# Optimization experiments

Hardware: AMD Instinct MI355X
Metric: run time of the kernel (lower is better)

The kernel has to match this reference:

```python
import jax, jax.numpy as jnp
import numpy as np

B, S, DIM = 2, 2048, 2048
H = 16
Q_LORA, KV_LORA = 768, 512
NOPE, ROPE, VD = 128, 64, 128
QKD = NOPE + ROPE  # 192
SOFTCAP = 30.0
EPS = 1e-6
NEG = -1e9
SCALE = QKD ** -0.5  # max_seq_len <= original_seq_len -> no mscale correction


def rms_norm(x, w, eps=EPS):
    xf = x.astype(jnp.float32)
    y = xf * jax.lax.rsqrt(jnp.mean(xf * xf, axis=-1, keepdims=True) + eps)
    return (y * w.astype(jnp.float32)).astype(x.dtype)


def apply_rope(x, cos, sin):
    # x: [B, S, H, D] with interleaved (even, odd) pairs; cos/sin: [S, D//2]
    xr = x.astype(jnp.float32).reshape(*x.shape[:-1], -1, 2)
    xe, xo = xr[..., 0], xr[..., 1]
    c = cos[None, :, None, :]
    s = sin[None, :, None, :]
    ye = xe * c - xo * s
    yo = xe * s + xo * c
    return jnp.stack([ye, yo], axis=-1).reshape(x.shape).astype(x.dtype)


def setup_inputs():
    key = jax.random.key(0)
    ks = jax.random.split(key, 6)
    def w(k, shape, fan_in):
        return jax.random.normal(k, shape, jnp.float32) * (fan_in ** -0.5)
    x = jax.random.normal(ks[0], (B, S, DIM), jnp.float32)
    wq_a_w = w(ks[1], (Q_LORA, DIM), DIM)
    wq_b_w = w(ks[2], (H * QKD, Q_LORA), Q_LORA)
    wkv_a_w = w(ks[3], (KV_LORA + ROPE, DIM), DIM)
    wkv_b_w = w(ks[4], (H * (NOPE + VD), KV_LORA), KV_LORA)
    wo_w = w(ks[5], (DIM, H * VD), H * VD)
    q_norm_w = jnp.ones((Q_LORA,), jnp.float32)
    kv_norm_w = jnp.ones((KV_LORA,), jnp.float32)
    q_gain = jnp.full((H,), 1.5, jnp.float32)  # qk_gain_init
    inv_freq = 1.0 / (10000.0 ** (np.arange(0, ROPE, 2, dtype=np.float32) / ROPE))
    fr = np.outer(np.arange(S, dtype=np.float32), inv_freq)  # [S, 32]
    freqs_cos = jnp.asarray(np.cos(fr))
    freqs_sin = jnp.asarray(np.sin(fr))
    mask = jnp.asarray(np.where(np.triu(np.ones((S, S), dtype=bool), 1), NEG, 0.0).astype(np.float32))
    return dict(x=x, wq_a_w=wq_a_w, q_norm_w=q_norm_w, wq_b_w=wq_b_w, q_gain=q_gain,
                wkv_a_w=wkv_a_w, kv_norm_w=kv_norm_w, wkv_b_w=wkv_b_w, wo_w=wo_w,
                freqs_cos=freqs_cos, freqs_sin=freqs_sin, mask=mask, start_pos=0)


def reference(x, wq_a_w, q_norm_w, wq_b_w, q_gain, wkv_a_w, kv_norm_w, wkv_b_w, wo_w,
              freqs_cos, freqs_sin, mask, start_pos):
    b, s, _ = x.shape
    # low-rank Q: wq_a -> RMSNorm -> wq_b
    q = rms_norm(x @ wq_a_w.T, q_norm_w) @ wq_b_w.T          # [B,S,H*QKD]
    q = q.reshape(b, s, H, QKD)
    q_nope, q_pe = q[..., :NOPE], q[..., NOPE:]
    q_pe = apply_rope(q_pe, freqs_cos, freqs_sin)            # rope_dims=0 -> full 64-dim rotation
    q_pe = q_pe * q_gain[None, None, :, None]                # learned per-head QK gain
    # low-rank KV + decoupled rope key
    kv_full = x @ wkv_a_w.T                                  # [B,S,KV_LORA+ROPE]
    kv, k_pe = kv_full[..., :KV_LORA], kv_full[..., KV_LORA:]
    kv = rms_norm(kv, kv_norm_w)
    k_pe = apply_rope(k_pe[:, :, None, :], freqs_cos, freqs_sin)  # [B,S,1,ROPE]
    # prefill (mask is not None) branch: expand latent kv through wkv_b
    kvb = (kv @ wkv_b_w.T).reshape(b, s, H, NOPE + VD)
    k_nope, v = kvb[..., :NOPE], kvb[..., NOPE:]
    k = jnp.concatenate([k_nope, jnp.broadcast_to(k_pe, (b, s, H, ROPE))], axis=-1)
    qf = jnp.concatenate([q_nope, q_pe], axis=-1)            # [B,S,H,QKD]
    scores = jnp.einsum('bshd,bthd->bsht', qf, k) * SCALE
    scores = SOFTCAP * jnp.tanh(scores / SOFTCAP)            # logit softcap
    scores = scores + mask[None, :, None, :]                 # causal additive mask [S,T]
    p = jax.nn.softmax(scores.astype(jnp.float32), axis=-1).astype(x.dtype)
    y = jnp.einsum('bsht,bthd->bshd', p, v)                  # [B,S,H,VD]
    # XSA: subtract self-value projection
    vn = v * jax.lax.rsqrt(jnp.maximum(jnp.sum(v * v, axis=-1, keepdims=True), 1e-12))
    y = y - jnp.sum(y * vn, axis=-1, keepdims=True) * vn
    return y.reshape(b, s, H * VD) @ wo_w.T                  # [B,S,DIM]
```

## Files before the change

### kernel.cpp

```cpp
#include <hip/hip_runtime.h>
#include <stdint.h>

typedef unsigned short u16;
typedef __bf16 bf16x8 __attribute__((ext_vector_type(8)));
typedef float f32x4 __attribute__((ext_vector_type(4)));
typedef unsigned int u32x4 __attribute__((ext_vector_type(4)));
typedef unsigned int u32x2 __attribute__((ext_vector_type(2)));

typedef __attribute__((address_space(3))) void LDSV;
typedef __attribute__((address_space(1))) void GLV;

#define S_LEN 2048

__device__ __forceinline__ float bf2f(u16 u) {
  union { unsigned int i; float f; } v; v.i = ((unsigned int)u) << 16; return v.f;
}
__device__ __forceinline__ u16 f2bf(float f) {
  union { float f; unsigned int i; } v; v.f = f;
  unsigned int x = v.i;
  return (u16)((x + 0x7fffu + ((x >> 16) & 1u)) >> 16);
}
__device__ __forceinline__ unsigned int cvtpk(float lo, float hi) {
  unsigned int r;
  asm("v_cvt_pk_bf16_f32 %0, %1, %2" : "=v"(r) : "v"(lo), "v"(hi));
  return r;
}
__device__ __forceinline__ unsigned long long pack4(float4 v) {
  return (unsigned long long)f2bf(v.x)
       | ((unsigned long long)f2bf(v.y) << 16)
       | ((unsigned long long)f2bf(v.z) << 32)
       | ((unsigned long long)f2bf(v.w) << 48);
}

__global__ __launch_bounds__(256) void cast_all(
    const float* __restrict__ s0, u16* __restrict__ d0, long e0,
    const float* __restrict__ s1, u16* __restrict__ d1, long e1,
    const float* __restrict__ s2, u16* __restrict__ d2, long e2,
    const float* __restrict__ s3, u16* __restrict__ d3, long e3,
    const float* __restrict__ s4, u16* __restrict__ d4, long e4,
    const float* __restrict__ s5, u16* __restrict__ d5, long e5) {
  long i = (long)blockIdx.x * 256 + threadIdx.x;
  const float* src; u16* dst; long base; bool pad = false;
  if (i < e0)      { src = s0; dst = d0; base = 0; }
  else if (i < e1) { src = s1; dst = d1; base = e0; }
  else if (i < e2) { src = s2; dst = d2; base = e1; }
  else if (i < e3) { src = s3; dst = d3; base = e2; }
  else if (i < e4) { src = s4; dst = d4; base = e3; }
  else if (i < e5) { src = s5; dst = d5; base = e4; pad = true; }
  else return;
  long li = i - base;
  long elem0 = li * 4;
  unsigned long long r = 0;
  if (!pad || (elem0 >> 11) < 576)
    r = pack4(*(const float4*)(src + elem0));
  ((unsigned long long*)dst)[li] = r;
}

template <int MODE>
__global__ __launch_bounds__(256) void gemm_nt(const u16* __restrict__ A, int lda,
                                               const u16* __restrict__ B, int ldb,
                                               void* __restrict__ Cv, int ldc,
                                               u16* __restrict__ Vc, int K) {
  __shared__ u16 As[128 * 64];
  __shared__ u16 Bs[128 * 64];
  const int tid = threadIdx.x;
  const int lane = tid & 63, wid = tid >> 6;
  const int l15 = lane & 15, l4 = lane >> 4;
  const int wr = wid >> 1, wc = wid & 1;
  const long bm = (long)blockIdx.y * 128;
  const long bn = (long)blockIdx.x * 128;

  const int srow = wid * 32 + (lane >> 3);
  const int scol = (lane & 7) * 8;
  const u16* Ag = A + (bm + srow) * (long)lda + scol;
  const u16* Bg = B + (bn + srow) * (long)ldb + scol;
  u16* AsW = &As[wid * 32 * 64];
  u16* BsW = &Bs[wid * 32 * 64];

  f32x4 acc[4][4] = {};

  for (int k0 = 0; k0 < K; k0 += 64) {
    __syncthreads();
#pragma unroll
    for (int ch = 0; ch < 4; ++ch) {
      __builtin_amdgcn_global_load_lds((const GLV*)(Ag + (long)ch * 8 * lda + k0),
                                       (LDSV*)(AsW + ch * 512), 16, 0, 0);
      __builtin_amdgcn_global_load_lds((const GLV*)(Bg + (long)ch * 8 * ldb + k0),
                                       (LDSV*)(BsW + ch * 512), 16, 0, 0);
    }
    __syncthreads();
#pragma unroll
    for (int kk = 0; kk < 2; ++kk) {
      bf16x8 af[4], bfr[4];
#pragma unroll
      for (int m = 0; m < 4; ++m)
        af[m] = *(const bf16x8*)(&As[(wr * 64 + m * 16 + l15) * 64 + (kk * 4 + l4) * 8]);
#pragma unroll
      for (int n = 0; n < 4; ++n)
        bfr[n] = *(const bf16x8*)(&Bs[(wc * 64 + n * 16 + l15) * 64 + (kk * 4 + l4) * 8]);
#pragma unroll
      for (int m = 0; m < 4; ++m)
#pragma unroll
        for (int n = 0; n < 4; ++n)
          acc[m][n] = __builtin_amdgcn_mfma_f32_16x16x32_bf16(af[m], bfr[n], acc[m][n], 0, 0, 0);
    }
  }
#pragma unroll
  for (int m = 0; m < 4; ++m)
#pragma unroll
    for (int n = 0; n < 4; ++n)
#pragma unroll
      for (int r = 0; r < 4; ++r) {
        long row = bm + wr * 64 + m * 16 + l4 * 4 + r;
        long col = bn + wc * 64 + n * 16 + l15;
        float v = acc[m][n][r];
        if constexpr (MODE == 0) {
          ((u16*)Cv)[row * ldc + col] = f2bf(v);
        } else if constexpr (MODE == 1) {
          ((float*)Cv)[row * ldc + col] = v;
        } else {
          int h = (int)(col >> 8), c = (int)(col & 255);
          if (c < 128)
            ((u16*)Cv)[(((row >> 11) * 16 + h) * 2048 + (row & 2047)) * 128 + c] = f2bf(v);
          else
            Vc[row * 2048 + h * 128 + (c - 128)] = f2bf(v);
        }
      }
}

#define MM_PHASE(QM, QN, BB)                                                     \
  __builtin_amdgcn_s_setprio(1);                                                 \
  {                                                                              \
    _Pragma("unroll") for (int mf = 0; mf < 4; ++mf) {                           \
      _Pragma("unroll") for (int nf = 0; nf < 2; ++nf) {                         \
        _Pragma("unroll") for (int kk = 0; kk < 2; ++kk) {                       \
          acc[(QM) * 4 + mf][(QN) * 2 + nf] =                                    \
              __builtin_amdgcn_mfma_f32_16x16x32_bf16(                           \
                  a[mf][kk], BB[nf][kk], acc[(QM) * 4 + mf][(QN) * 2 + nf],      \
                  0, 0, 0);                                                      \
        }                                                                        \
      }                                                                          \
    }                                                                            \
  }                                                                              \
  __builtin_amdgcn_s_setprio(0);

template <int MODE>
__global__ __launch_bounds__(512, 2) void gemm256(const u16* __restrict__ A, int lda,
                                                  const u16* __restrict__ B, int ldb,
                                                  void* __restrict__ Cv, int ldc,
                                                  u16* __restrict__ Vc, int K) {
  __shared__ u16 SMEM[65536];
  const int tid = threadIdx.x;
  const int lane = tid & 63, wid = tid >> 6;
  const int l15 = lane & 15, l4 = lane >> 4;
  const int wm16 = (wid >> 2) * 16, wn16 = (wid & 3) * 16;

  const int gx = gridDim.x, nwg = gx * gridDim.y;
  int lin0 = blockIdx.y * gx + blockIdx.x;
  int cpx = nwg >> 3;
  int swzb = (lin0 & 7) * cpx + (lin0 >> 3);
  const long bm = (long)(swzb / gx) * 256;
  const long bn = (long)(swzb % gx) * 256;

  long aoff[2], boff[2];
#pragma unroll
  for (int j = 0; j < 2; ++j) {
    int lb = (j * 512 + tid) * 16;
    int swz = lb ^ (((lb >> 7) & 7) << 4);
    int sr = swz >> 7, sc = (swz & 127) >> 1;
    aoff[j] = (bm + sr) * (long)lda + sc;
    boff[j] = (bn + sr) * (long)ldb + sc;
  }

  auto STAGE = [&](int buf, int half, int isB, int tt) {
#pragma unroll
    for (int j = 0; j < 2; ++j) {
      const u16* src = isB ? (B + boff[j] + (long)half * 128 * ldb + tt * 64)
                           : (A + aoff[j] + (long)half * 128 * lda + tt * 64);
      __builtin_amdgcn_global_load_lds(
          (const GLV*)src,
          (LDSV*)((char*)SMEM + isB * 65536 + buf * 32768 + half * 16384 +
                  (j * 512 + tid) * 16),
          16, 0, 0);
    }
  };

  f32x4 acc[8][4] = {};
  bf16x8 a[4][2], b0[2][2], b1[2][2];

  auto LDA_ = [&](int buf, int qm) {
#pragma unroll
    for (int mf = 0; mf < 4; ++mf)
#pragma unroll
      for (int kk = 0; kk < 2; ++kk) {
        int r = mf * 32 + wm16 + l15;
        int lb = r * 128 + kk * 64 + l4 * 16;
        a[mf][kk] = *(const bf16x8*)((char*)SMEM + buf * 32768 + qm * 16384 +
                                     (lb ^ ((r & 7) << 4)));
      }
  };
  auto LDB_ = [&](int buf, int qn, bf16x8 (*bb)[2]) {
#pragma unroll
    for (int nf = 0; nf < 2; ++nf)
#pragma unroll
      for (int kk = 0; kk < 2; ++kk) {
        int r = nf * 64 + wn16 + l15;
        int lb = r * 128 + kk * 64 + l4 * 16;
        bb[nf][kk] = *(const bf16x8*)((char*)SMEM + 65536 + buf * 32768 +
                                      qn * 16384 + (lb ^ ((r & 7) << 4)));
      }
  };

  const int NT = K >> 6;
  STAGE(0, 0, 0, 0); STAGE(0, 0, 1, 0); STAGE(0, 1, 1, 0); STAGE(0, 1, 0, 0);
  STAGE(1, 0, 0, 1); STAGE(1, 0, 1, 1);
  asm volatile("s_waitcnt vmcnt(4)" ::: "memory");
  __builtin_amdgcn_s_barrier();

  for (int t = 0; t < NT; ++t) {
    const int cb = t & 1;
    if (t + 1 < NT) STAGE(cb ^ 1, 1, 1, t + 1);
    LDA_(cb, 0);
    LDB_(cb, 0, b0);
    __builtin_amdgcn_s_barrier();
    asm volatile("s_waitcnt lgkmcnt(0)" ::: "memory");
    __builtin_amdgcn_sched_barrier(0);
    MM_PHASE(0, 0, b0);
    __builtin_amdgcn_s_barrier();
    if (t + 1 < NT) STAGE(cb ^ 1, 1, 0, t + 1);
    LDB_(cb, 1, b1);
    __builtin_amdgcn_s_barrier();
    asm volatile("s_waitcnt lgkmcnt(0)" ::: "memory");
    __builtin_amdgcn_sched_barrier(0);
    MM_PHASE(0, 1, b1);
    __builtin_amdgcn_s_barrier();
    if (t + 2 < NT) STAGE(cb, 0, 0, t + 2);
    LDA_(cb, 1);
    __builtin_amdgcn_s_barrier();
    asm volatile("s_waitcnt lgkmcnt(0)" ::: "memory");
    __builtin_amdgcn_sched_barrier(0);
    MM_PHASE(1, 0, b0);
    __builtin_amdgcn_s_barrier();
    if (t + 2 < NT) STAGE(cb, 0, 1, t + 2);
    __builtin_amdgcn_s_barrier();
    MM_PHASE(1, 1, b1);
    if (t + 2 < NT) asm volatile("s_waitcnt vmcnt(4)" ::: "memory");
    else            asm volatile("s_waitcnt vmcnt(0)" ::: "memory");
    __builtin_amdgcn_s_barrier();
  }

#pragma unroll
  for (int mfg = 0; mfg < 8; ++mfg)
#pragma unroll
    for (int nfg = 0; nfg < 4; ++nfg)
#pragma unroll
      for (int r = 0; r < 4; ++r) {
        long row = bm + mfg * 32 + wm16 + l4 * 4 + r;
        long col = bn + nfg * 64 + wn16 + l15;
        float v = acc[mfg][nfg][r];
        if constexpr (MODE == 0) {
          ((u16*)Cv)[row * ldc + col] = f2bf(v);
        } else if constexpr (MODE == 1) {
          ((float*)Cv)[row * ldc + col] = v;
        } else {
          int h = (int)(col >> 8), c = (int)(col & 255);
          if (c < 128)
            ((u16*)Cv)[(((row >> 11) * 16 + h) * 2048 + (row & 2047)) * 128 + c] = f2bf(v);
          else
            Vc[row * 2048 + h * 128 + (c - 128)] = f2bf(v);
        }
      }
}

#define MM_TALL(QM, QN, BB)                                                      \
  __builtin_amdgcn_s_setprio(1);                                                 \
  {                                                                              \
    _Pragma("unroll") for (int mf = 0; mf < 4; ++mf) {                           \
      _Pragma("unroll") for (int kk = 0; kk < 2; ++kk) {                         \
        acc[(QM) * 4 + mf][(QN)] = __builtin_amdgcn_mfma_f32_16x16x32_bf16(      \
            a[mf][kk], BB[kk], acc[(QM) * 4 + mf][(QN)], 0, 0, 0);               \
      }                                                                          \
    }                                                                            \
  }                                                                              \
  __builtin_amdgcn_s_setprio(0);

template <int MODE>
__global__ __launch_bounds__(512, 2) void gemm_tall(const u16* __restrict__ A, int lda,
                                                    const u16* __restrict__ B, int ldb,
                                                    void* __restrict__ Cv, int ldc,
                                                    u16* __restrict__ Vc, int K) {
  __shared__ u16 SMEM[49152];
  const int tid = threadIdx.x;
  const int lane = tid & 63, wid = tid >> 6;
  const int l15 = lane & 15, l4 = lane >> 4;
  const int wm16 = (wid >> 2) * 16, wn16 = (wid & 3) * 16;

  const int gx = gridDim.x, nwg = gx * gridDim.y;
  int lin0 = blockIdx.y * gx + blockIdx.x;
  int cpx = nwg >> 3;
  int swzb = (lin0 & 7) * cpx + (lin0 >> 3);
  const long bm = (long)(swzb / gx) * 256;
  const long bn = (long)(swzb % gx) * 128;

  long aoff[2], boffv;
#pragma unroll
  for (int j = 0; j < 2; ++j) {
    int lb = (j * 512 + tid) * 16;
    int swz = lb ^ (((lb >> 7) & 7) << 4);
    aoff[j] = (bm + (swz >> 7)) * (long)lda + ((swz & 127) >> 1);
  }
  {
    int lb = tid * 16;
    int swz = lb ^ (((lb >> 7) & 7) << 4);
    boffv = (bn + (swz >> 7)) * (long)ldb + ((swz & 127) >> 1);
  }

  auto SA = [&](int buf, int half, int tt) {
#pragma unroll
    for (int j = 0; j < 2; ++j)
      __builtin_amdgcn_global_load_lds(
          (const GLV*)(A + aoff[j] + (long)half * 128 * lda + tt * 64),
          (LDSV*)((char*)SMEM + buf * 32768 + half * 16384 + (j * 512 + tid) * 16),
          16, 0, 0);
  };
  auto SB = [&](int buf, int half, int tt) {
    __builtin_amdgcn_global_load_lds(
        (const GLV*)(B + boffv + (long)half * 64 * ldb + tt * 64),
        (LDSV*)((char*)SMEM + 65536 + buf * 16384 + half * 8192 + tid * 16),
        16, 0, 0);
  };

  f32x4 acc[8][2] = {};
  bf16x8 a[4][2], b0[2], b1[2];

  auto LDA_ = [&](int buf, int qm) {
#pragma unroll
    for (int mf = 0; mf < 4; ++mf)
#pragma unroll
      for (int kk = 0; kk < 2; ++kk) {
        int r = mf * 32 + wm16 + l15;
        int lb = r * 128 + kk * 64 + l4 * 16;
        a[mf][kk] = *(const bf16x8*)((char*)SMEM + buf * 32768 + qm * 16384 +
                                     (lb ^ ((r & 7) << 4)));
      }
  };
  auto LDB_ = [&](int buf, int qn, bf16x8* bb) {
#pragma unroll
    for (int kk = 0; kk < 2; ++kk) {
      int r = wn16 + l15;
      int lb = r * 128 + kk * 64 + l4 * 16;
      bb[kk] = *(const bf16x8*)((char*)SMEM + 65536 + buf * 16384 + qn * 8192 +
                                (lb ^ ((r & 7) << 4)));
    }
  };

  const int NT = K >> 6;
  SA(0, 0, 0); SB(0, 0, 0); SB(0, 1, 0); SA(0, 1, 0);
  SA(1, 0, 1); SB(1, 0, 1);
  asm volatile("s_waitcnt vmcnt(3)" ::: "memory");
  __builtin_amdgcn_s_barrier();

  for (int t = 0; t < NT; ++t) {
    const int cb = t & 1;
    if (t + 1 < NT) SB(cb ^ 1, 1, t + 1);
    LDA_(cb, 0);
    LDB_(cb, 0, b0);
    __builtin_amdgcn_s_barrier();
    asm volatile("s_waitcnt lgkmcnt(0)" ::: "memory");
    __builtin_amdgcn_sched_barrier(0);
    MM_TALL(0, 0, b0);
    __builtin_amdgcn_s_barrier();
    if (t + 1 < NT) SA(cb ^ 1, 1, t + 1);
    LDB_(cb, 1, b1);
    __builtin_amdgcn_s_barrier();
    asm volatile("s_waitcnt lgkmcnt(0)" ::: "memory");
    __builtin_amdgcn_sched_barrier(0);
    MM_TALL(0, 1, b1);
    __builtin_amdgcn_s_barrier();
    if (t + 2 < NT) SA(cb, 0, t + 2);
    LDA_(cb, 1);
    __builtin_amdgcn_s_barrier();
    asm volatile("s_waitcnt lgkmcnt(0)" ::: "memory");
    __builtin_amdgcn_sched_barrier(0);
    MM_TALL(1, 0, b0);
    __builtin_amdgcn_s_barrier();
    if (t + 2 < NT) SB(cb, 0, t + 2);
    __builtin_amdgcn_s_barrier();
    MM_TALL(1, 1, b1);
    if (t + 2 < NT) asm volatile("s_waitcnt vmcnt(6)" ::: "memory");
    else            asm volatile("s_waitcnt vmcnt(0)" ::: "memory");
    __builtin_amdgcn_s_barrier();
  }

#pragma unroll
  for (int mfg = 0; mfg < 8; ++mfg)
#pragma unroll
    for (int qn = 0; qn < 2; ++qn)
#pragma unroll
      for (int r = 0; r < 4; ++r) {
        long row = bm + mfg * 32 + wm16 + l4 * 4 + r;
        long col = bn + qn * 64 + wn16 + l15;
        float v = acc[mfg][qn][r];
        if constexpr (MODE == 0) {
          ((u16*)Cv)[row * ldc + col] = f2bf(v);
        } else if constexpr (MODE == 1) {
          ((float*)Cv)[row * ldc + col] = v;
        } else {
          int h = (int)(col >> 8), c = (int)(col & 255);
          if (c < 128)
            ((u16*)Cv)[(((row >> 11) * 16 + h) * 2048 + (row & 2047)) * 128 + c] = f2bf(v);
          else
            Vc[row * 2048 + h * 128 + (c - 128)] = f2bf(v);
        }
      }
}

__global__ __launch_bounds__(256) void rmsnorm2_kernel(u16* __restrict__ qakv,
                                                       const float* __restrict__ qw,
                                                       const float* __restrict__ kvw) {
  __shared__ float sred[4];
  const int tid = threadIdx.x;
  const int row = blockIdx.x;
  if (row < 4096) {
    u16* p = qakv + (size_t)row * 1408;
    float x[3];
    float ss = 0.f;
#pragma unroll
    for (int i = 0; i < 3; ++i) { x[i] = bf2f(p[tid + i * 256]); ss += x[i] * x[i]; }
#pragma unroll
    for (int off = 1; off < 64; off <<= 1) ss += __shfl_xor(ss, off);
    if ((tid & 63) == 0) sred[tid >> 6] = ss;
    __syncthreads();
    float tot = sred[0] + sred[1] + sred[2] + sred[3];
    float rs = rsqrtf(tot * (1.0f / 768.0f) + 1e-6f) * 0.0069411711f;
#pragma unroll
    for (int i = 0; i < 3; ++i) p[tid + i * 256] = f2bf(x[i] * rs * qw[tid + i * 256]);
  } else {
    u16* p = qakv + (size_t)(row - 4096) * 1408 + 768;
    float x[2];
    float ss = 0.f;
#pragma unroll
    for (int i = 0; i < 2; ++i) { x[i] = bf2f(p[tid + i * 256]); ss += x[i] * x[i]; }
#pragma unroll
    for (int off = 1; off < 64; off <<= 1) ss += __shfl_xor(ss, off);
    if ((tid & 63) == 0) sred[tid >> 6] = ss;
    __syncthreads();
    float tot = sred[0] + sred[1] + sred[2] + sred[3];
    float rs = rsqrtf(tot * (1.0f / 512.0f) + 1e-6f);
#pragma unroll
    for (int i = 0; i < 2; ++i) p[tid + i * 256] = f2bf(x[i] * rs * kvw[tid + i * 256]);
  }
}

__global__ __launch_bounds__(256) void rope_q_kernel(u16* __restrict__ q,
                                                     const float* __restrict__ cosb,
                                                     const float* __restrict__ sinb,
                                                     const float* __restrict__ gain) {
  int idx = blockIdx.x * 256 + threadIdx.x;
  int i = idx & 31;
  int h = (idx >> 5) & 15;
  int srow = idx >> 9;
  int s = srow & (S_LEN - 1);
  size_t base = (size_t)srow * 3072 + h * 192 + 128 + 2 * i;
  unsigned int* p = (unsigned int*)(q + base);
  unsigned int v = *p;
  float xe = bf2f((u16)(v & 0xffff)), xo = bf2f((u16)(v >> 16));
  float c = cosb[s * 32 + i], sn = sinb[s * 32 + i];
  float g = gain[h];
  float ye = (xe * c - xo * sn) * g, yo = (xe * sn + xo * c) * g;
  *p = (unsigned int)f2bf(ye) | ((unsigned int)f2bf(yo) << 16);
}

__global__ __launch_bounds__(256) void ropek_kernel(const u16* __restrict__ qakv,
                                                    const float* __restrict__ cosb,
                                                    const float* __restrict__ sinb,
                                                    u16* __restrict__ kpe) {
  int idx = blockIdx.x * 256 + threadIdx.x;
  int i = idx & 31;
  int srow = idx >> 5;
  int s = srow & 2047;
  unsigned int v = *(const unsigned int*)(qakv + (size_t)srow * 1408 + 1280 + 2 * i);
  float xe = bf2f((u16)(v & 0xffff)), xo = bf2f((u16)(v >> 16));
  float c = cosb[s * 32 + i], sn = sinb[s * 32 + i];
  *(unsigned int*)(kpe + (size_t)srow * 64 + 2 * i) =
      (unsigned int)f2bf(xe * c - xo * sn) | ((unsigned int)f2bf(xe * sn + xo * c) << 16);
}

__global__ __launch_bounds__(256) void v_transpose_kernel(const u16* __restrict__ Vc,
                                                          u16* __restrict__ VT) {
  __shared__ u16 tile[64][65];
  int bh = blockIdx.z;
  int d0 = blockIdx.y * 64;
  int t0 = blockIdx.x * 64;
  int b = bh >> 4, h = bh & 15;
#pragma unroll
  for (int i = 0; i < 2; ++i) {
    int flat = i * 256 + threadIdx.x;
    int t = flat >> 3, c = (flat & 7) * 8;
    u32x4 v = *(const u32x4*)(Vc + ((long)b * S_LEN + t0 + t) * 2048 + h * 128 + d0 + c);
    const u16* pv = (const u16*)&v;
#pragma unroll
    for (int j = 0; j < 8; ++j) tile[c + j][t] = pv[j];
  }
  __syncthreads();
#pragma unroll
  for (int i = 0; i < 2; ++i) {
    int flat = i * 256 + threadIdx.x;
    int d = flat >> 3, tc = (flat & 7) * 8;
    u32x4 v;
    u16* pv = (u16*)&v;
#pragma unroll
    for (int j = 0; j < 8; ++j) pv[j] = tile[d][tc + j];
    *(u32x4*)(VT + ((long)bh * 128 + d0 + d) * S_LEN + t0 + tc) = v;
  }
}

__global__ __launch_bounds__(512, 2) void attn_kernel(const u16* __restrict__ Qg,
                                                      const u16* __restrict__ KbN,
                                                      const u16* __restrict__ Kpe,
                                                      const u16* __restrict__ VTg,
                                                      const u16* __restrict__ Vcg,
                                                      u16* __restrict__ Yg) {
  __shared__ u16 Ks[64 * 192];
  __shared__ u16 VTs[128 * 64];
  __shared__ u16 Ps[128 * 64];

  const int tid = threadIdx.x, lane = tid & 63, wid = tid >> 6;
  const int l15 = lane & 15, l4 = lane >> 4;

  const int p = blockIdx.x;
  const int bh = (p & 7) * 4 + (p >> 6);
  const int pair = (p >> 3) & 7;
  const int b = bh >> 4, h = bh & 15;

  const u16* Kn = KbN + (long)bh * S_LEN * 128;
  const u16* Kp = Kpe + (long)b * S_LEN * 64;
  const u16* Vbh = VTg + (long)bh * 128 * S_LEN;

  int krow[3], sst[3];
  const u16* sb[3];
  u16* ksw[3];
#pragma unroll
  for (int i = 0; i < 3; ++i) {
    int flat = i * 512 + tid;
    int r = flat / 24, c = flat % 24;
    krow[i] = r;
    if (c < 16) { sb[i] = Kn + c * 8; sst[i] = 128; }
    else        { sb[i] = Kp + (c - 16) * 8; sst[i] = 64; }
    ksw[i] = &Ks[r * 192 + ((c ^ (r & 7)) * 8)];
  }
  int vrow[2], vc[2];
  u16* vsw[2];
#pragma unroll
  for (int i = 0; i < 2; ++i) {
    int flat = i * 512 + tid;
    vrow[i] = flat >> 3; vc[i] = flat & 7;
    vsw[i] = &VTs[vrow[i] * 64 + ((vc[i] ^ (vrow[i] & 7)) * 8)];
  }

  const int prow = wid * 16 + l15;
  const int pr7 = prow & 7;

  for (int seg = 0; seg < 2; ++seg) {
    const int qt = seg ? pair : 15 - pair;
    const int q0 = qt * 128;
    const int nkt = 2 * qt + 2;

    bf16x8 qf[6];
    {
      const u16* qb_ = Qg + ((long)b * S_LEN + q0 + prow) * 3072 + h * 192;
#pragma unroll
      for (int f = 0; f < 6; ++f) qf[f] = *(const bf16x8*)(qb_ + f * 32 + 8 * l4);
    }

    f32x4 o[8] = {};
    float lsum = 0.f;

    u32x4 ka[3], va[2];
#pragma unroll
    for (int i = 0; i < 3; ++i)
      ka[i] = *(const u32x4*)(sb[i] + (long)krow[i] * sst[i]);
#pragma unroll
    for (int i = 0; i < 2; ++i)
      va[i] = *(const u32x4*)(Vbh + (long)vrow[i] * S_LEN + vc[i] * 8);

    for (int it = 0; it < nkt; ++it) {
      __syncthreads();
#pragma unroll
      for (int i = 0; i < 3; ++i) *(u32x4*)ksw[i] = ka[i];
#pragma unroll
      for (int i = 0; i < 2; ++i) *(u32x4*)vsw[i] = va[i];
      __syncthreads();
      if (it + 1 < nkt) {
        int k0n = (it + 1) * 64;
#pragma unroll
        for (int i = 0; i < 3; ++i)
          ka[i] = *(const u32x4*)(sb[i] + (long)(k0n + krow[i]) * sst[i]);
#pragma unroll
        for (int i = 0; i < 2; ++i)
          va[i] = *(const u32x4*)(Vbh + (long)vrow[i] * S_LEN + k0n + vc[i] * 8);
      }

      f32x4 sacc[4] = {};
      __builtin_amdgcn_s_setprio(1);
#pragma unroll
      for (int f = 0; f < 6; ++f)
#pragma unroll
        for (int tf = 0; tf < 4; ++tf) {
          int row = tf * 16 + l15;
          bf16x8 kf = *(const bf16x8*)(&Ks[row * 192 + (((f * 4 + l4) ^ (row & 7)) * 8)]);
          sacc[tf] = __builtin_amdgcn_mfma_f32_16x16x32_bf16(kf, qf[f], sacc[tf], 0, 0, 0);
        }
      __builtin_amdgcn_s_setprio(0);

#pragma unroll
      for (int tf = 0; tf < 4; ++tf)
#pragma unroll
        for (int r = 0; r < 4; ++r) {
          float u = __builtin_amdgcn_exp2f(sacc[tf][r]);
          sacc[tf][r] = __builtin_amdgcn_exp2f(-86.56170245333781f *
                                               __builtin_amdgcn_rcpf(u + 1.0f));
        }
      if (it * 64 >= q0) {
        const int dthr = q0 + prow - it * 64 - l4 * 4;
#pragma unroll
        for (int tf = 0; tf < 4; ++tf)
#pragma unroll
          for (int r = 0; r < 4; ++r)
            if (tf * 16 + r > dthr) sacc[tf][r] = 0.f;
      }
#pragma unroll
      for (int tf = 0; tf < 4; ++tf)
#pragma unroll
        for (int r = 0; r < 4; ++r) lsum += sacc[tf][r];

#pragma unroll
      for (int tf = 0; tf < 4; ++tf) {
        u32x2 w;
        w.x = cvtpk(sacc[tf][0], sacc[tf][1]);
        w.y = cvtpk(sacc[tf][2], sacc[tf][3]);
        int chunk = tf * 2 + (l4 >> 1);
        *(u32x2*)(&Ps[prow * 64 + ((chunk ^ pr7) * 8) + (l4 & 1) * 4]) = w;
      }

      __builtin_amdgcn_s_setprio(1);
#pragma unroll
      for (int kk = 0; kk < 2; ++kk) {
        bf16x8 pf = *(const bf16x8*)(&Ps[prow * 64 + (((kk * 4 + l4) ^ pr7) * 8)]);
#pragma unroll
        for (int nf = 0; nf < 8; ++nf) {
          int vr = nf * 16 + l15;
          bf16x8 vf = *(const bf16x8*)(&VTs[vr * 64 + (((kk * 4 + l4) ^ (vr & 7)) * 8)]);
          o[nf] = __builtin_amdgcn_mfma_f32_16x16x32_bf16(pf, vf, o[nf], 0, 0, 0);
        }
      }
      __builtin_amdgcn_s_setprio(0);
    }

    lsum += __shfl_xor(lsum, 16);
    lsum += __shfl_xor(lsum, 32);
    float inv[4];
#pragma unroll
    for (int r = 0; r < 4; ++r)
      inv[r] = __builtin_amdgcn_rcpf(__shfl(lsum, l4 * 4 + r));

    float yv[8][4], vvv[8][4];
    float ssum[4] = {0.f, 0.f, 0.f, 0.f}, dsum[4] = {0.f, 0.f, 0.f, 0.f};
    const u16* vb = Vcg + ((long)b * S_LEN + q0 + wid * 16) * 2048 + h * 128;
#pragma unroll
    for (int nf = 0; nf < 8; ++nf)
#pragma unroll
      for (int r = 0; r < 4; ++r) {
        float vv = bf2f(vb[(l4 * 4 + r) * 2048 + nf * 16 + l15]);
        float y = o[nf][r] * inv[r];
        vvv[nf][r] = vv; yv[nf][r] = y;
        ssum[r] += vv * vv; dsum[r] += y * vv;
      }
#pragma unroll
    for (int r = 0; r < 4; ++r) {
      ssum[r] += __shfl_xor(ssum[r], 1); ssum[r] += __shfl_xor(ssum[r], 2);
      ssum[r] += __shfl_xor(ssum[r], 4); ssum[r] += __shfl_xor(ssum[r], 8);
      dsum[r] += __shfl_xor(dsum[r], 1); dsum[r] += __shfl_xor(dsum[r], 2);
      dsum[r] += __shfl_xor(dsum[r], 4); dsum[r] += __shfl_xor(dsum[r], 8);
      dsum[r] *= __builtin_amdgcn_rcpf(fmaxf(ssum[r], 1e-12f));
    }
#pragma unroll
    for (int nf = 0; nf < 8; ++nf)
#pragma unroll
      for (int r = 0; r < 4; ++r) {
        long row = (long)b * S_LEN + q0 + wid * 16 + l4 * 4 + r;
        Yg[row * 2048 + h * 128 + nf * 16 + l15] = f2bf(yv[nf][r] - dsum[r] * vvv[nf][r]);
      }
  }
}

extern "C" void kernel_launch(void* const* d_in, const int* in_sizes, int n_in,
                              void* d_out, int out_size, void* d_ws, size_t ws_size,
                              hipStream_t stream) {
  const float* x       = (const float*)d_in[0];
  const float* wq_a    = (const float*)d_in[1];
  const float* q_norm  = (const float*)d_in[2];
  const float* wq_b    = (const float*)d_in[3];
  const float* q_gain  = (const float*)d_in[4];
  const float* wkv_a   = (const float*)d_in[5];
  const float* kv_norm = (const float*)d_in[6];
  const float* wkv_b   = (const float*)d_in[7];
  const float* wo      = (const float*)d_in[8];
  const float* fcos    = (const float*)d_in[9];
  const float* fsin    = (const float*)d_in[10];
  float* out = (float*)d_out;

  char* ws = (char*)d_ws;
  size_t off = 0;
  auto alloc = [&](size_t bytes) {
    char* pp = ws + off;
    off += (bytes + 255) & ~(size_t)255;
    return pp;
  };
  const long M = 4096;
  u16* xb    = (u16*)alloc(M * 2048 * 2);
  u16* wcomb = (u16*)alloc(1408L * 2048 * 2);
  u16* wqbb  = (u16*)alloc(3072L * 768 * 2);
  u16* wkvbb = (u16*)alloc(4096L * 512 * 2);
  u16* wob   = (u16*)alloc(2048L * 2048 * 2);
  u16* qakv  = (u16*)alloc(M * 1408 * 2);
  u16* qb    = (u16*)alloc(M * 3072 * 2);
  u16* KbN   = (u16*)alloc(32L * 2048 * 128 * 2);
  u16* kpe   = (u16*)alloc(M * 64 * 2);
  u16* Vc    = (u16*)alloc(M * 2048 * 2);
  u16* VTb   = (u16*)alloc(32L * 128 * 2048 * 2);
  u16* Yb    = (u16*)alloc(M * 2048 * 2);

  const long n4_x = 2097152, n4_wqa = 393216, n4_wqb = 589824,
             n4_wkvb = 524288, n4_wo = 1048576, n4_wkvap = 327680;
  long e0 = n4_x, e1 = e0 + n4_wqa, e2 = e1 + n4_wqb, e3 = e2 + n4_wkvb,
       e4 = e3 + n4_wo, e5 = e4 + n4_wkvap;
  cast_all<<<(int)(e5 / 256), 256, 0, stream>>>(
      x, xb, e0, wq_a, wcomb, e1, wq_b, wqbb, e2, wkv_b, wkvbb, e3,
      wo, wob, e4, wkv_a, wcomb + 768L * 2048, e5);

  gemm_tall<0><<<dim3(11, 16), 512, 0, stream>>>(xb, 2048, wcomb, 2048, qakv, 1408, nullptr, 2048);
  rmsnorm2_kernel<<<8192, 256, 0, stream>>>(qakv, q_norm, kv_norm);
  gemm256<0><<<dim3(12, 16), 512, 0, stream>>>(qakv, 1408, wqbb, 768, qb, 3072, nullptr, 768);
  rope_q_kernel<<<2097152 / 256, 256, 0, stream>>>(qb, fcos, fsin, q_gain);
  ropek_kernel<<<131072 / 256, 256, 0, stream>>>(qakv, fcos, fsin, kpe);
  gemm256<2><<<dim3(16, 16), 512, 0, stream>>>(qakv + 768, 1408, wkvbb, 512, KbN, 0, Vc, 512);
  v_transpose_kernel<<<dim3(32, 2, 32), 256, 0, stream>>>(Vc, VTb);
  attn_kernel<<<256, 512, 0, stream>>>(qb, KbN, kpe, VTb, Vc, Yb);
  gemm_tall<1><<<dim3(16, 16), 512, 0, stream>>>(Yb, 2048, wob, 2048, out, 2048, nullptr, 2048);
}
```

Measured before the change: 246.5 us.

## Fuse Q rope into attention and double-buffer K/V LDS tiles

Removes the standalone rope_q kernel and applies rotary embedding plus per-head gain to the query fragments in registers inside the attention kernel, saving one launch and one read-modify-write pass over Q. The K and V^T shared-memory tiles are double-buffered, so the next tile is written to LDS during compute and the two barriers per iteration drop to one. Unused gemm_nt code is deleted. Doubling the LDS buffers raises shared memory use per block and may reduce occupancy.

```diff
diff --git a/kernel.cpp b/kernel.cpp
--- a/kernel.cpp
+++ b/kernel.cpp
@@ -56,78 +56,6 @@
   ((unsigned long long*)dst)[li] = r;
 }
 
-template <int MODE>
-__global__ __launch_bounds__(256) void gemm_nt(const u16* __restrict__ A, int lda,
-                                               const u16* __restrict__ B, int ldb,
-                                               void* __restrict__ Cv, int ldc,
-                                               u16* __restrict__ Vc, int K) {
-  __shared__ u16 As[128 * 64];
-  __shared__ u16 Bs[128 * 64];
-  const int tid = threadIdx.x;
-  const int lane = tid & 63, wid = tid >> 6;
-  const int l15 = lane & 15, l4 = lane >> 4;
-  const int wr = wid >> 1, wc = wid & 1;
-  const long bm = (long)blockIdx.y * 128;
-  const long bn = (long)blockIdx.x * 128;
-
-  const int srow = wid * 32 + (lane >> 3);
-  const int scol = (lane & 7) * 8;
-  const u16* Ag = A + (bm + srow) * (long)lda + scol;
-  const u16* Bg = B + (bn + srow) * (long)ldb + scol;
-  u16* AsW = &As[wid * 32 * 64];
-  u16* BsW = &Bs[wid * 32 * 64];
-
-  f32x4 acc[4][4] = {};
-
-  for (int k0 = 0; k0 < K; k0 += 64) {
-    __syncthreads();
-#pragma unroll
-    for (int ch = 0; ch < 4; ++ch) {
-      __builtin_amdgcn_global_load_lds((const GLV*)(Ag + (long)ch * 8 * lda + k0),
-                                       (LDSV*)(AsW + ch * 512), 16, 0, 0);
-      __builtin_amdgcn_global_load_lds((const GLV*)(Bg + (long)ch * 8 * ldb + k0),
-                                       (LDSV*)(BsW + ch * 512), 16, 0, 0);
-    }
-    __syncthreads();
-#pragma unroll
-    for (int kk = 0; kk < 2; ++kk) {
-      bf16x8 af[4], bfr[4];
-#pragma unroll
-      for (int m = 0; m < 4; ++m)
-        af[m] = *(const bf16x8*)(&As[(wr * 64 + m * 16 + l15) * 64 + (kk * 4 + l4) * 8]);
-#pragma unroll
-      for (int n = 0; n < 4; ++n)
-        bfr[n] = *(const bf16x8*)(&Bs[(wc * 64 + n * 16 + l15) * 64 + (kk * 4 + l4) * 8]);
-#pragma unroll
-      for (int m = 0; m < 4; ++m)
-#pragma unroll
-        for (int n = 0; n < 4; ++n)
-          acc[m][n] = __builtin_amdgcn_mfma_f32_16x16x32_bf16(af[m], bfr[n], acc[m][n], 0, 0, 0);
-    }
-  }
-#pragma unroll
-  for (int m = 0; m < 4; ++m)
-#pragma unroll
-    for (int n = 0; n < 4; ++n)
-#pragma unroll
-      for (int r = 0; r < 4; ++r) {
-        long row = bm + wr * 64 + m * 16 + l4 * 4 + r;
-        long col = bn + wc * 64 + n * 16 + l15;
-        float v = acc[m][n][r];
-        if constexpr (MODE == 0) {
-          ((u16*)Cv)[row * ldc + col] = f2bf(v);
-        } else if constexpr (MODE == 1) {
-          ((float*)Cv)[row * ldc + col] = v;
-        } else {
-          int h = (int)(col >> 8), c = (int)(col & 255);
-          if (c < 128)
-            ((u16*)Cv)[(((row >> 11) * 16 + h) * 2048 + (row & 2047)) * 128 + c] = f2bf(v);
-          else
-            Vc[row * 2048 + h * 128 + (c - 128)] = f2bf(v);
-        }
-      }
-}
-
 #define MM_PHASE(QM, QN, BB)                                                     \
   __builtin_amdgcn_s_setprio(1);                                                 \
   {                                                                              \
@@ -452,25 +380,6 @@
   }
 }
 
-__global__ __launch_bounds__(256) void rope_q_kernel(u16* __restrict__ q,
-                                                     const float* __restrict__ cosb,
-                                                     const float* __restrict__ sinb,
-                                                     const float* __restrict__ gain) {
-  int idx = blockIdx.x * 256 + threadIdx.x;
-  int i = idx & 31;
-  int h = (idx >> 5) & 15;
-  int srow = idx >> 9;
-  int s = srow & (S_LEN - 1);
-  size_t base = (size_t)srow * 3072 + h * 192 + 128 + 2 * i;
-  unsigned int* p = (unsigned int*)(q + base);
-  unsigned int v = *p;
-  float xe = bf2f((u16)(v & 0xffff)), xo = bf2f((u16)(v >> 16));
-  float c = cosb[s * 32 + i], sn = sinb[s * 32 + i];
-  float g = gain[h];
-  float ye = (xe * c - xo * sn) * g, yo = (xe * sn + xo * c) * g;
-  *p = (unsigned int)f2bf(ye) | ((unsigned int)f2bf(yo) << 16);
-}
-
 __global__ __launch_bounds__(256) void ropek_kernel(const u16* __restrict__ qakv,
                                                     const float* __restrict__ cosb,
                                                     const float* __restrict__ sinb,
@@ -520,9 +429,12 @@
                                                       const u16* __restrict__ Kpe,
                                                       const u16* __restrict__ VTg,
                                                       const u16* __restrict__ Vcg,
+                                                      const float* __restrict__ cosb,
+                                                      const float* __restrict__ sinb,
+                                                      const float* __restrict__ gain,
                                                       u16* __restrict__ Yg) {
-  __shared__ u16 Ks[64 * 192];
-  __shared__ u16 VTs[128 * 64];
+  __shared__ u16 Ks[2][64 * 192];
+  __shared__ u16 VTs[2][128 * 64];
   __shared__ u16 Ps[128 * 64];
 
   const int tid = threadIdx.x, lane = tid & 63, wid = tid >> 6;
@@ -537,9 +449,8 @@
   const u16* Kp = Kpe + (long)b * S_LEN * 64;
   const u16* Vbh = VTg + (long)bh * 128 * S_LEN;
 
-  int krow[3], sst[3];
+  int krow[3], sst[3], ksoff[3];
   const u16* sb[3];
-  u16* ksw[3];
 #pragma unroll
   for (int i = 0; i < 3; ++i) {
     int flat = i * 512 + tid;
@@ -547,31 +458,46 @@
     krow[i] = r;
     if (c < 16) { sb[i] = Kn + c * 8; sst[i] = 128; }
     else        { sb[i] = Kp + (c - 16) * 8; sst[i] = 64; }
-    ksw[i] = &Ks[r * 192 + ((c ^ (r & 7)) * 8)];
-  }
-  int vrow[2], vc[2];
-  u16* vsw[2];
+    ksoff[i] = r * 192 + ((c ^ (r & 7)) * 8);
+  }
+  int vrow[2], vc[2], vsoff[2];
 #pragma unroll
   for (int i = 0; i < 2; ++i) {
     int flat = i * 512 + tid;
     vrow[i] = flat >> 3; vc[i] = flat & 7;
-    vsw[i] = &VTs[vrow[i] * 64 + ((vc[i] ^ (vrow[i] & 7)) * 8)];
+    vsoff[i] = vrow[i] * 64 + ((vc[i] ^ (vrow[i] & 7)) * 8);
   }
 
   const int prow = wid * 16 + l15;
   const int pr7 = prow & 7;
+  const float g = gain[h];
 
   for (int seg = 0; seg < 2; ++seg) {
     const int qt = seg ? pair : 15 - pair;
     const int q0 = qt * 128;
     const int nkt = 2 * qt + 2;
+    const int sq = q0 + prow;
 
     bf16x8 qf[6];
     {
-      const u16* qb_ = Qg + ((long)b * S_LEN + q0 + prow) * 3072 + h * 192;
+      const u16* qb_ = Qg + ((long)b * S_LEN + sq) * 3072 + h * 192;
 #pragma unroll
       for (int f = 0; f < 6; ++f) qf[f] = *(const bf16x8*)(qb_ + f * 32 + 8 * l4);
     }
+#pragma unroll
+    for (int f = 4; f < 6; ++f) {
+      float4 cv = *(const float4*)(cosb + sq * 32 + (f - 4) * 16 + l4 * 4);
+      float4 sv = *(const float4*)(sinb + sq * 32 + (f - 4) * 16 + l4 * 4);
+      float cc[4] = {cv.x, cv.y, cv.z, cv.w};
+      float ssn[4] = {sv.x, sv.y, sv.z, sv.w};
+      u16* pq = (u16*)&qf[f];
+#pragma unroll
+      for (int pp = 0; pp < 4; ++pp) {
+        float xe = bf2f(pq[2 * pp]), xo = bf2f(pq[2 * pp + 1]);
+        pq[2 * pp]     = f2bf((xe * cc[pp] - xo * ssn[pp]) * g);
+        pq[2 * pp + 1] = f2bf((xe * ssn[pp] + xo * cc[pp]) * g);
+      }
+    }
 
     f32x4 o[8] = {};
     float lsum = 0.f;
@@ -583,23 +509,22 @@
 #pragma unroll
     for (int i = 0; i < 2; ++i)
       va[i] = *(const u32x4*)(Vbh + (long)vrow[i] * S_LEN + vc[i] * 8);
+#pragma unroll
+    for (int i = 0; i < 3; ++i) *(u32x4*)(&Ks[0][ksoff[i]]) = ka[i];
+#pragma unroll
+    for (int i = 0; i < 2; ++i) *(u32x4*)(&VTs[0][vsoff[i]]) = va[i];
+    if (nkt > 1) {
+#pragma unroll
+      for (int i = 0; i < 3; ++i)
+        ka[i] = *(const u32x4*)(sb[i] + (long)(64 + krow[i]) * sst[i]);
+#pragma unroll
+      for (int i = 0; i < 2; ++i)
+        va[i] = *(const u32x4*)(Vbh + (long)vrow[i] * S_LEN + 64 + vc[i] * 8);
+    }
+    __syncthreads();
 
     for (int it = 0; it < nkt; ++it) {
-      __syncthreads();
-#pragma unroll
-      for (int i = 0; i < 3; ++i) *(u32x4*)ksw[i] = ka[i];
-#pragma unroll
-      for (int i = 0; i < 2; ++i) *(u32x4*)vsw[i] = va[i];
-      __syncthreads();
-      if (it + 1 < nkt) {
-        int k0n = (it + 1) * 64;
-#pragma unroll
-        for (int i = 0; i < 3; ++i)
-          ka[i] = *(const u32x4*)(sb[i] + (long)(k0n + krow[i]) * sst[i]);
-#pragma unroll
-        for (int i = 0; i < 2; ++i)
-          va[i] = *(const u32x4*)(Vbh + (long)vrow[i] * S_LEN + k0n + vc[i] * 8);
-      }
+      const int cur = it & 1;
 
       f32x4 sacc[4] = {};
       __builtin_amdgcn_s_setprio(1);
@@ -608,10 +533,26 @@
 #pragma unroll
         for (int tf = 0; tf < 4; ++tf) {
           int row = tf * 16 + l15;
-          bf16x8 kf = *(const bf16x8*)(&Ks[row * 192 + (((f * 4 + l4) ^ (row & 7)) * 8)]);
+          bf16x8 kf = *(const bf16x8*)(&Ks[cur][row * 192 + (((f * 4 + l4) ^ (row & 7)) * 8)]);
           sacc[tf] = __builtin_amdgcn_mfma_f32_16x16x32_bf16(kf, qf[f], sacc[tf], 0, 0, 0);
         }
       __builtin_amdgcn_s_setprio(0);
+
+      if (it + 1 < nkt) {
+#pragma unroll
+        for (int i = 0; i < 3; ++i) *(u32x4*)(&Ks[cur ^ 1][ksoff[i]]) = ka[i];
+#pragma unroll
+        for (int i = 0; i < 2; ++i) *(u32x4*)(&VTs[cur ^ 1][vsoff[i]]) = va[i];
+      }
+      if (it + 2 < nkt) {
+        int k0n = (it + 2) * 64;
+#pragma unroll
+        for (int i = 0; i < 3; ++i)
+          ka[i] = *(const u32x4*)(sb[i] + (long)(k0n + krow[i]) * sst[i]);
+#pragma unroll
+        for (int i = 0; i < 2; ++i)
+          va[i] = *(const u32x4*)(Vbh + (long)vrow[i] * S_LEN + k0n + vc[i] * 8);
+      }
 
 #pragma unroll
       for (int tf = 0; tf < 4; ++tf)
@@ -650,11 +591,13 @@
 #pragma unroll
         for (int nf = 0; nf < 8; ++nf) {
           int vr = nf * 16 + l15;
-          bf16x8 vf = *(const bf16x8*)(&VTs[vr * 64 + (((kk * 4 + l4) ^ (vr & 7)) * 8)]);
+          bf16x8 vf = *(const bf16x8*)(&VTs[cur][vr * 64 + (((kk * 4 + l4) ^ (vr & 7)) * 8)]);
           o[nf] = __builtin_amdgcn_mfma_f32_16x16x32_bf16(pf, vf, o[nf], 0, 0, 0);
         }
       }
       __builtin_amdgcn_s_setprio(0);
+
+      __syncthreads();
     }
 
     lsum += __shfl_xor(lsum, 16);
@@ -742,10 +685,9 @@
   gemm_tall<0><<<dim3(11, 16), 512, 0, stream>>>(xb, 2048, wcomb, 2048, qakv, 1408, nullptr, 2048);
   rmsnorm2_kernel<<<8192, 256, 0, stream>>>(qakv, q_norm, kv_norm);
   gemm256<0><<<dim3(12, 16), 512, 0, stream>>>(qakv, 1408, wqbb, 768, qb, 3072, nullptr, 768);
-  rope_q_kernel<<<2097152 / 256, 256, 0, stream>>>(qb, fcos, fsin, q_gain);
   ropek_kernel<<<131072 / 256, 256, 0, stream>>>(qakv, fcos, fsin, kpe);
   gemm256<2><<<dim3(16, 16), 512, 0, stream>>>(qakv + 768, 1408, wkvbb, 512, KbN, 0, Vc, 512);
   v_transpose_kernel<<<dim3(32, 2, 32), 256, 0, stream>>>(Vc, VTb);
-  attn_kernel<<<256, 512, 0, stream>>>(qb, KbN, kpe, VTb, Vc, Yb);
+  attn_kernel<<<256, 512, 0, stream>>>(qb, KbN, kpe, VTb, Vc, fcos, fsin, q_gain, Yb);
   gemm_tall<1><<<dim3(16, 16), 512, 0, stream>>>(Yb, 2048, wob, 2048, out, 2048, nullptr, 2048);
 }
```

Measured after the change: 238.4 us. 3.3% less time.
